# Performance work log

Hardware: AMD Instinct MI355X
Metric: run time of the kernel (lower is better)

The kernel has to match this reference:

```python
import jax, jax.numpy as jnp
import numpy as np


def setup_inputs() -> dict:
    key = jax.random.key(0)
    k1, k2 = jax.random.split(key)
    B, T, K, D = 8, 4096, 1024, 256
    x = jax.random.normal(k1, (B, T, D), dtype=jnp.float32)
    codebook = jax.random.normal(k2, (K, D), dtype=jnp.float32)
    return {"x": x, "codebook": codebook}


def reference(x, codebook):
    # Faithful to: dist = tf.norm(z_e - lookup_, axis=-1); argmin(dist, -1).
    # argmin of the Euclidean norm == argmin of the squared distance, so we
    # instead of materializing the (B, T, k, d) broadcast intermediate.
    x2 = jnp.sum(x * x, axis=-1, keepdims=True)          # (B, T, 1)
    c2 = jnp.sum(codebook * codebook, axis=-1)           # (k,)
    xc = jnp.einsum('btd,kd->btk', x, codebook)          # (B, T, k)
    dist2 = x2 + c2 - 2.0 * xc                           # (B, T, k)
    return jnp.argmin(dist2, axis=-1)                    # (B, T) int
```

## Files before the change

### kernel.cpp

```cpp
#include <hip/hip_runtime.h>
#include <stdint.h>

typedef __attribute__((ext_vector_type(8))) _Float16 f16x8;
typedef __attribute__((ext_vector_type(4))) float f32x4;

#define MARG 0.09375f

__device__ __forceinline__ void glds16(const void* g, void* l) {
  __builtin_amdgcn_global_load_lds(
      (const __attribute__((address_space(1))) void*)g,
      (__attribute__((address_space(3))) void*)l, 16, 0, 0);
}

__device__ __forceinline__ unsigned short f2h(float f) {
  return __builtin_bit_cast(unsigned short, (_Float16)f);
}

__global__ __launch_bounds__(256) void vq_prep_cb(const float* __restrict__ cb,
                                                  unsigned short* __restrict__ cbh,
                                                  float* __restrict__ hc,
                                                  float* __restrict__ cbT,
                                                  int* __restrict__ count) {
  __shared__ float tile[16][260];
  const int tid = threadIdx.x;
  const int r0 = blockIdx.x * 16;
  const int lane = tid & 63;
  const int wave = tid >> 6;

#pragma unroll
  for (int i = 0; i < 4; ++i) {
    int r = i * 4 + (tid >> 6);
    int d = lane * 4;
    float4 v = *reinterpret_cast<const float4*>(cb + (size_t)(r0 + r) * 256 + d);
    *reinterpret_cast<float4*>(&tile[r][d]) = v;
    ushort4 h;
    h.x = f2h(v.x); h.y = f2h(v.y); h.z = f2h(v.z); h.w = f2h(v.w);
    *reinterpret_cast<ushort4*>(cbh + (size_t)(r0 + r) * 256 + d) = h;
  }
  __syncthreads();

#pragma unroll
  for (int i = 0; i < 4; ++i) {
    int r = wave * 4 + i;
    float4 v = *reinterpret_cast<const float4*>(&tile[r][lane * 4]);
    float s = v.x * v.x + v.y * v.y + v.z * v.z + v.w * v.w;
#pragma unroll
    for (int m = 32; m >= 1; m >>= 1) s += __shfl_xor(s, m, 64);
    if (lane == 0) hc[r0 + r] = 0.5f * s;
  }

  {
    const int d = tid;
#pragma unroll
    for (int i = 0; i < 4; ++i) {
      float4 v = make_float4(tile[i * 4 + 0][d], tile[i * 4 + 1][d],
                             tile[i * 4 + 2][d], tile[i * 4 + 3][d]);
      *reinterpret_cast<float4*>(cbT + (size_t)d * 1024 + r0 + i * 4) = v;
    }
  }
  if (blockIdx.x == 0 && tid == 0) *count = 0;
}

__global__ __launch_bounds__(512, 4) void vq_mfma_kernel(
    const float* __restrict__ x, const unsigned short* __restrict__ cbh,
    const float* __restrict__ hc, int* __restrict__ out,
    int* __restrict__ list, int* __restrict__ count) {
  __shared__ unsigned short Alds[16384];
  __shared__ unsigned short Blds[16384];
  __shared__ float c2s[1024];
  __shared__ float cbv[4][64];
  __shared__ int   cbi[4][64];
  __shared__ float csv[4][64];

  const int tid = threadIdx.x;
  const int lane = tid & 63;
  const int wave = tid >> 6;
  const int wr = wave >> 2;
  const int wc = wave & 3;
  const int l15 = lane & 15;
  const int l4  = lane >> 4;
  const int bswz = (blockIdx.x & 7) * 64 + (blockIdx.x >> 3);
  const int r0 = bswz * 64;

  reinterpret_cast<float2*>(c2s)[tid] = reinterpret_cast<const float2*>(hc)[tid];

  {
    const int row = tid >> 3;
    const int cc  = tid & 7;
    const float* src = x + (size_t)(r0 + row) * 256 + cc * 32;
    unsigned short hv[32];
#pragma unroll
    for (int q = 0; q < 8; ++q) {
      float4 v = *reinterpret_cast<const float4*>(src + q * 4);
      hv[q * 4 + 0] = f2h(v.x); hv[q * 4 + 1] = f2h(v.y);
      hv[q * 4 + 2] = f2h(v.z); hv[q * 4 + 3] = f2h(v.w);
    }
    char* base = reinterpret_cast<char*>(Alds);
#pragma unroll
    for (int g = 0; g < 4; ++g) {
      int byte = (row * 512 + cc * 64 + g * 16) ^ ((row & 7) << 4);
      *reinterpret_cast<f16x8*>(base + byte) = *reinterpret_cast<const f16x8*>(&hv[g * 8]);
    }
  }

  auto stage = [&](int T1) {
    const int p = T1 & 1;
    const int n0 = (T1 >> 3) << 8;
    const int d0 = (T1 & 7) << 5;
    unsigned short* B = Blds + p * 8192;
#pragma unroll
    for (int r = 0; r < 2; ++r) {
      int idx = r * 512 + tid;
      int bch = (idx & 3) ^ ((idx >> 3) & 3);
      glds16(cbh + (size_t)(n0 + (idx >> 2)) * 256 + d0 + bch * 8, B + idx * 8);
    }
  };

  float bestv[2][4], secondv[2][4];
  int besti[2][4];
#pragma unroll
  for (int tr = 0; tr < 2; ++tr)
#pragma unroll
    for (int g = 0; g < 4; ++g) {
      bestv[tr][g] = -3.4e38f; secondv[tr][g] = -3.4e38f; besti[tr][g] = 0;
    }

  __syncthreads();
  stage(0);

  const int swzf = (l15 >> 1) & 3;
  int abase[2];
#pragma unroll
  for (int tr = 0; tr < 2; ++tr) {
    int arow = wr * 32 + tr * 16 + l15;
    abase[tr] = (arow * 512 + l4 * 16) ^ ((arow & 7) << 4);
  }

  int T = 0;
  for (int nt = 0; nt < 4; ++nt) {
    f32x4 acc[2][4];
#pragma unroll
    for (int tr = 0; tr < 2; ++tr)
#pragma unroll
      for (int tc = 0; tc < 4; ++tc) acc[tr][tc] = (f32x4){0.f, 0.f, 0.f, 0.f};

    for (int dt = 0; dt < 8; ++dt, ++T) {
      const int p = T & 1;
      if (T < 31) {
        stage(T + 1);
        asm volatile("s_waitcnt vmcnt(2)" ::: "memory");
      } else {
        asm volatile("s_waitcnt vmcnt(0)" ::: "memory");
      }
      __builtin_amdgcn_s_barrier();

      const char* Ab = reinterpret_cast<const char*>(Alds);
      const unsigned short* B = Blds + p * 8192;

      f16x8 af[2], bf[4];
#pragma unroll
      for (int tr = 0; tr < 2; ++tr)
        af[tr] = *reinterpret_cast<const f16x8*>(Ab + (abase[tr] ^ (dt * 64)));
#pragma unroll
      for (int tc = 0; tc < 4; ++tc) {
        int bcol = wc * 64 + tc * 16 + l15;
        bf[tc] = *reinterpret_cast<const f16x8*>(B + bcol * 32 + (l4 ^ swzf) * 8);
      }

#pragma unroll
      for (int tr = 0; tr < 2; ++tr)
#pragma unroll
        for (int tc = 0; tc < 4; ++tc)
          acc[tr][tc] = __builtin_amdgcn_mfma_f32_16x16x32_f16(af[tr], bf[tc], acc[tr][tc], 0, 0, 0);

      asm volatile("s_waitcnt lgkmcnt(0)" ::: "memory");
      __builtin_amdgcn_s_barrier();
    }

    const int cb0 = nt * 256 + wc * 64 + l15;
    float hcv[4];
#pragma unroll
    for (int tc = 0; tc < 4; ++tc) hcv[tc] = c2s[cb0 + tc * 16];
#pragma unroll
    for (int tr = 0; tr < 2; ++tr)
#pragma unroll
      for (int tc = 0; tc < 4; ++tc) {
        const int code = cb0 + tc * 16;
#pragma unroll
        for (int g = 0; g < 4; ++g) {
          float s = acc[tr][tc][g] - hcv[tc];
          bool gt = s > bestv[tr][g];
          float ns = gt ? bestv[tr][g] : fmaxf(secondv[tr][g], s);
          bestv[tr][g] = gt ? s : bestv[tr][g];
          besti[tr][g] = gt ? code : besti[tr][g];
          secondv[tr][g] = ns;
        }
      }
  }

#pragma unroll
  for (int tr = 0; tr < 2; ++tr)
#pragma unroll
    for (int g = 0; g < 4; ++g) {
      float bv = bestv[tr][g]; int bi = besti[tr][g]; float sv = secondv[tr][g];
#pragma unroll
      for (int m = 1; m < 16; m <<= 1) {
        float ov = __shfl_xor(bv, m, 64);
        int   oi = __shfl_xor(bi, m, 64);
        float os = __shfl_xor(sv, m, 64);
        sv = fmaxf(fmaxf(sv, os), fminf(bv, ov));
        bool gt = (ov > bv) || (ov == bv && oi < bi);
        bv = gt ? ov : bv;
        bi = gt ? oi : bi;
      }
      if (l15 == 0) {
        int rl = wr * 32 + tr * 16 + l4 * 4 + g;
        cbv[wc][rl] = bv; cbi[wc][rl] = bi; csv[wc][rl] = sv;
      }
    }

  __syncthreads();
  if (tid < 64) {
    float bv = cbv[0][tid]; int bi = cbi[0][tid]; float sv = csv[0][tid];
#pragma unroll
    for (int w2 = 1; w2 < 4; ++w2) {
      float ov = cbv[w2][tid]; int oi = cbi[w2][tid]; float os = csv[w2][tid];
      sv = fmaxf(fmaxf(sv, os), fminf(bv, ov));
      bool gt = (ov > bv) || (ov == bv && oi < bi);
      bv = gt ? ov : bv;
      bi = gt ? oi : bi;
    }
    out[r0 + tid] = bi;
    if (sv >= bv - MARG) {
      int slot = atomicAdd(count, 1);
      list[slot] = r0 + tid;
    }
  }
}

__global__ __launch_bounds__(512) void vq_cleanup(const float* __restrict__ x,
                                                  const float* __restrict__ cbT,
                                                  const float* __restrict__ hc,
                                                  const int* __restrict__ list,
                                                  const int* __restrict__ count,
                                                  int* __restrict__ out) {
  __shared__ float xt[4][256];
  __shared__ int rowids[4];
  __shared__ float wbv[8][2];
  __shared__ int   wbi[8][2];
  const int tid = threadIdx.x;
  const int wave = tid >> 6;
  const int half = tid >> 8;
  const int c0 = (tid & 255) * 4;
  const int n = *count;

  for (int t0 = blockIdx.x * 4; t0 < n; t0 += gridDim.x * 4) {
    __syncthreads();
    if (tid < 4) rowids[tid] = (t0 + tid < n) ? list[t0 + tid] : -1;
    __syncthreads();
    {
      int j = tid >> 7, seg = tid & 127;
      int row = rowids[j];
      if (row < 0) row = rowids[0];
      *reinterpret_cast<float2*>(&xt[j][seg * 2]) =
          *reinterpret_cast<const float2*>(x + (size_t)row * 256 + seg * 2);
    }
    __syncthreads();

    float a0[4], a1[4];
#pragma unroll
    for (int k = 0; k < 4; ++k) { a0[k] = 0.f; a1[k] = 0.f; }

    const float4* cvp = reinterpret_cast<const float4*>(cbT) + (c0 >> 2);
    const float* xr0 = &xt[half * 2 + 0][0];
    const float* xr1 = &xt[half * 2 + 1][0];
#pragma unroll 4
    for (int d = 0; d < 256; ++d) {
      float4 cv = cvp[d * 256];
      float x0 = xr0[d];
      float x1 = xr1[d];
      a0[0] = fmaf(cv.x, x0, a0[0]); a0[1] = fmaf(cv.y, x0, a0[1]);
      a0[2] = fmaf(cv.z, x0, a0[2]); a0[3] = fmaf(cv.w, x0, a0[3]);
      a1[0] = fmaf(cv.x, x1, a1[0]); a1[1] = fmaf(cv.y, x1, a1[1]);
      a1[2] = fmaf(cv.z, x1, a1[2]); a1[3] = fmaf(cv.w, x1, a1[3]);
    }

    float4 hcv = *reinterpret_cast<const float4*>(hc + c0);

#pragma unroll
    for (int r = 0; r < 2; ++r) {
      const float* a = (r == 0) ? a0 : a1;
      float bv = a[0] - hcv.x; int bi = c0;
      float s1 = a[1] - hcv.y; if (s1 > bv) { bv = s1; bi = c0 + 1; }
      float s2 = a[2] - hcv.z; if (s2 > bv) { bv = s2; bi = c0 + 2; }
      float s3 = a[3] - hcv.w; if (s3 > bv) { bv = s3; bi = c0 + 3; }
#pragma unroll
      for (int m = 1; m < 64; m <<= 1) {
        float ov = __shfl_xor(bv, m, 64);
        int   oi = __shfl_xor(bi, m, 64);
        bool gt = (ov > bv) || (ov == bv && oi < bi);
        bv = gt ? ov : bv;
        bi = gt ? oi : bi;
      }
      if ((tid & 63) == 0) { wbv[wave][r] = bv; wbi[wave][r] = bi; }
    }
    __syncthreads();
    if (tid < 4 && rowids[tid] >= 0) {
      int h2 = tid >> 1, lr = tid & 1;
      int wbase = h2 * 4;
      float bv = wbv[wbase][lr]; int bi = wbi[wbase][lr];
#pragma unroll
      for (int w2 = 1; w2 < 4; ++w2) {
        float ov = wbv[wbase + w2][lr]; int oi = wbi[wbase + w2][lr];
        if (ov > bv || (ov == bv && oi < bi)) { bv = ov; bi = oi; }
      }
      out[rowids[tid]] = bi;
    }
  }
}

#define BM 128
#define BN 256
#define BD 32
#define NT 512

__global__ __launch_bounds__(256) void vq_c2_kernel(const float* __restrict__ cb,
                                                    float* __restrict__ halfc2) {
  int row  = blockIdx.x * 4 + (threadIdx.x >> 6);
  int lane = threadIdx.x & 63;
  float4 v = *reinterpret_cast<const float4*>(cb + (size_t)row * 256 + lane * 4);
  float s = v.x * v.x + v.y * v.y + v.z * v.z + v.w * v.w;
#pragma unroll
  for (int m = 32; m >= 1; m >>= 1) s += __shfl_xor(s, m, 64);
  if (lane == 0) halfc2[row] = 0.5f * s;
}

__global__ __launch_bounds__(NT, 2) void vq_argmin_kernel(
    const float* __restrict__ x, const float* __restrict__ cb,
    const float* __restrict__ halfc2, int* __restrict__ out) {
  __shared__ float lds[2][(BM + BN) * BD];
  __shared__ float c2s[1024];
  const int tid = threadIdx.x;
  const int w   = tid >> 6;
  const int tc  = tid & 31;
  const int tr  = tid >> 5;
  const int r0  = blockIdx.x * BM;
  reinterpret_cast<float2*>(c2s)[tid] = reinterpret_cast<const float2*>(halfc2)[tid];
  const int sA  = tr & 7;
  const int sB  = tc & 7;
  const int sAB = sA ^ sB;
  const int cho = (((tid & 7) ^ w)) * 4;
  const int sub = tid >> 3;
  float bestv[8]; int besti[8];
#pragma unroll
  for (int i = 0; i < 8; ++i) { bestv[i] = -3.4e38f; besti[i] = 0; }
  auto stage = [&](int n0, int d0, int p) {
    float* dst  = &lds[p][0];
    float* dstB = dst + BM * BD;
#pragma unroll
    for (int r = 0; r < 2; ++r) {
      int t2 = r * NT + tid;
      glds16(x + (size_t)(r0 + r * 64 + sub) * 256 + d0 + cho, dst + t2 * 4);
    }
#pragma unroll
    for (int r = 0; r < 4; ++r) {
      int t2 = r * NT + tid;
      glds16(cb + (size_t)(n0 + r * 64 + sub) * 256 + d0 + cho, dstB + t2 * 4);
    }
  };
  stage(0, 0, 0);
  int t = 0;
  for (int nt = 0; nt < 4; ++nt) {
    float acc[8][8];
#pragma unroll
    for (int i = 0; i < 8; ++i)
#pragma unroll
      for (int j = 0; j < 8; ++j) acc[i][j] = 0.f;
    for (int dt = 0; dt < 8; ++dt, ++t) {
      const int p = t & 1;
      if (t < 31) {
        const int t1 = t + 1;
        stage((t1 >> 3) * BN, (t1 & 7) * BD, t1 & 1);
        asm volatile("s_waitcnt vmcnt(6)" ::: "memory");
      } else {
        asm volatile("s_waitcnt vmcnt(0)" ::: "memory");
      }
      __builtin_amdgcn_s_barrier();
      const float* pA = &lds[p][tr * 8 * BD];
      const float* pB = &lds[p][BM * BD + tc * 8 * BD];
#pragma unroll
      for (int cc = 0; cc < 8; ++cc) {
        const float* pBc = pB + ((cc ^ sAB) << 2);
        float4 a[8], b[8];
#pragma unroll
        for (int i = 0; i < 8; ++i)
          a[i] = *reinterpret_cast<const float4*>(pA + i * BD + cc * 4);
#pragma unroll
        for (int j = 0; j < 8; ++j)
          b[j] = *reinterpret_cast<const float4*>(pBc + j * BD);
#pragma unroll
        for (int i = 0; i < 8; ++i)
#pragma unroll
          for (int j = 0; j < 8; ++j) {
            acc[i][j] = fmaf(a[i].x, b[j].x, acc[i][j]);
            acc[i][j] = fmaf(a[i].y, b[j].y, acc[i][j]);
            acc[i][j] = fmaf(a[i].z, b[j].z, acc[i][j]);
            acc[i][j] = fmaf(a[i].w, b[j].w, acc[i][j]);
          }
      }
      asm volatile("s_waitcnt lgkmcnt(0)" ::: "memory");
      __builtin_amdgcn_s_barrier();
    }
    const int n0 = nt * BN;
#pragma unroll
    for (int j = 0; j < 8; ++j) {
      const int code = n0 + tc * 8 + j;
      const float hc = c2s[code];
#pragma unroll
      for (int i = 0; i < 8; ++i) {
        float s = acc[i][j] - hc;
        if (s > bestv[i]) { bestv[i] = s; besti[i] = code; }
      }
    }
  }
#pragma unroll
  for (int i = 0; i < 8; ++i) {
#pragma unroll
    for (int m = 1; m <= 16; m <<= 1) {
      float ov = __shfl_xor(bestv[i], m, 64);
      int   oi = __shfl_xor(besti[i], m, 64);
      if (ov > bestv[i] || (ov == bestv[i] && oi < besti[i])) { bestv[i] = ov; besti[i] = oi; }
    }
  }
  if (tc == 0) {
#pragma unroll
    for (int i = 0; i < 8; ++i) out[r0 + tr * 8 + i] = besti[i];
  }
}

extern "C" void kernel_launch(void* const* d_in, const int* in_sizes, int n_in,
                              void* d_out, int out_size, void* d_ws, size_t ws_size,
                              hipStream_t stream) {
  const float* x  = (const float*)d_in[0];
  const float* cb = (const float*)d_in[1];
  int* out = (int*)d_out;

  const size_t OFF_CH  = 0;
  const size_t OFF_HC  = OFF_CH + (size_t)1024 * 256 * 2;
  const size_t OFF_CBT = OFF_HC + (size_t)1024 * 4;
  const size_t OFF_LS  = OFF_CBT + (size_t)1024 * 256 * 4;
  const size_t OFF_CT  = OFF_LS + (size_t)32768 * 4;
  const size_t NEED    = OFF_CT + 64;

  if (ws_size >= NEED) {
    unsigned short* cbh = (unsigned short*)((char*)d_ws + OFF_CH);
    float* hc  = (float*)((char*)d_ws + OFF_HC);
    float* cbT = (float*)((char*)d_ws + OFF_CBT);
    int* list  = (int*)((char*)d_ws + OFF_LS);
    int* count = (int*)((char*)d_ws + OFF_CT);

    hipLaunchKernelGGL(vq_prep_cb, dim3(64), dim3(256), 0, stream, cb, cbh, hc, cbT, count);
    hipLaunchKernelGGL(vq_mfma_kernel, dim3(512), dim3(512), 0, stream,
                       x, cbh, hc, out, list, count);
    hipLaunchKernelGGL(vq_cleanup, dim3(1024), dim3(512), 0, stream,
                       x, cbT, hc, list, count, out);
  } else {
    float* c2 = (float*)d_ws;
    hipLaunchKernelGGL(vq_c2_kernel, dim3(256), dim3(256), 0, stream, cb, c2);
    hipLaunchKernelGGL(vq_argmin_kernel, dim3(32768 / BM), dim3(NT), 0, stream,
                       x, cb, c2, out);
  }
}
```

Before: 68.56 us.

## Give each wave a private codebook slice to drop per-step block barriers

Restructures the MFMA kernel so every wave handles all 64 rows against its own 128-code slice of the codebook, streamed into a per-wave double-buffered LDS region. Because each wave consumes only the data it staged itself, the two block-wide barriers per k-step go away and only vmcnt waits remain. The A tile is stored pre-fragmented in an MFMA-friendly layout, and the final reduction now merges eight waves instead of four. The catch is that each wave now reads more A fragments from LDS, register pressure rises (launch bounds drop to 2), and the fully unrolled loop grows code size.

```diff
diff --git a/kernel.cpp b/kernel.cpp
--- a/kernel.cpp
+++ b/kernel.cpp
@@ -61,22 +61,20 @@
   if (blockIdx.x == 0 && tid == 0) *count = 0;
 }
 
-__global__ __launch_bounds__(512, 4) void vq_mfma_kernel(
+__global__ __launch_bounds__(512, 2) void vq_mfma_kernel(
     const float* __restrict__ x, const unsigned short* __restrict__ cbh,
     const float* __restrict__ hc, int* __restrict__ out,
     int* __restrict__ list, int* __restrict__ count) {
   __shared__ unsigned short Alds[16384];
-  __shared__ unsigned short Blds[16384];
+  __shared__ unsigned short Bpriv[16384];
   __shared__ float c2s[1024];
-  __shared__ float cbv[4][64];
-  __shared__ int   cbi[4][64];
-  __shared__ float csv[4][64];
+  __shared__ float cbv[8][64];
+  __shared__ int   cbi[8][64];
+  __shared__ float csv[8][64];
 
   const int tid = threadIdx.x;
   const int lane = tid & 63;
   const int wave = tid >> 6;
-  const int wr = wave >> 2;
-  const int wc = wave & 3;
   const int l15 = lane & 15;
   const int l4  = lane >> 4;
   const int bswz = (blockIdx.x & 7) * 64 + (blockIdx.x >> 3);
@@ -96,113 +94,99 @@
       hv[q * 4 + 2] = f2h(v.z); hv[q * 4 + 3] = f2h(v.w);
     }
     char* base = reinterpret_cast<char*>(Alds);
+    const int rt = row >> 4, rl = row & 15;
+#pragma unroll
+    for (int j8 = 0; j8 < 4; ++j8) {
+      int byte = (rt * 8 + cc) * 1024 + j8 * 256 + rl * 16;
+      *reinterpret_cast<f16x8*>(base + byte) = *reinterpret_cast<const f16x8*>(&hv[j8 * 8]);
+    }
+  }
+  __syncthreads();
+
+  const char* Ab = reinterpret_cast<const char*>(Alds);
+  const int laneb = lane * 16;
+  char* Bw = reinterpret_cast<char*>(Bpriv) + wave * 4096;
+  const int cw0 = wave * 128;
+  const int bro = (l15 * 4 + l4) * 16;
+
+  auto stage = [&](int T) {
+    const int n0 = cw0 + ((T >> 3) << 5);
+    const int d0 = (T & 7) << 5;
+    char* dst = Bw + (T & 1) * 2048;
+    const unsigned short* s0 = cbh + (size_t)(n0 + (lane >> 2)) * 256 + d0 + ((lane & 3) << 3);
+    glds16(s0, dst + lane * 16);
+    glds16(s0 + 16 * 256, dst + 1024 + lane * 16);
+  };
+
+  float bestv[4][4], secv[4][4];
+  int besti[4][4];
+#pragma unroll
+  for (int rt = 0; rt < 4; ++rt)
 #pragma unroll
     for (int g = 0; g < 4; ++g) {
-      int byte = (row * 512 + cc * 64 + g * 16) ^ ((row & 7) << 4);
-      *reinterpret_cast<f16x8*>(base + byte) = *reinterpret_cast<const f16x8*>(&hv[g * 8]);
-    }
-  }
-
-  auto stage = [&](int T1) {
-    const int p = T1 & 1;
-    const int n0 = (T1 >> 3) << 8;
-    const int d0 = (T1 & 7) << 5;
-    unsigned short* B = Blds + p * 8192;
-#pragma unroll
-    for (int r = 0; r < 2; ++r) {
-      int idx = r * 512 + tid;
-      int bch = (idx & 3) ^ ((idx >> 3) & 3);
-      glds16(cbh + (size_t)(n0 + (idx >> 2)) * 256 + d0 + bch * 8, B + idx * 8);
-    }
-  };
-
-  float bestv[2][4], secondv[2][4];
-  int besti[2][4];
-#pragma unroll
-  for (int tr = 0; tr < 2; ++tr)
-#pragma unroll
-    for (int g = 0; g < 4; ++g) {
-      bestv[tr][g] = -3.4e38f; secondv[tr][g] = -3.4e38f; besti[tr][g] = 0;
-    }
-
-  __syncthreads();
+      bestv[rt][g] = -3.4e38f; secv[rt][g] = -3.4e38f; besti[rt][g] = 0;
+    }
+
   stage(0);
 
-  const int swzf = (l15 >> 1) & 3;
-  int abase[2];
-#pragma unroll
-  for (int tr = 0; tr < 2; ++tr) {
-    int arow = wr * 32 + tr * 16 + l15;
-    abase[tr] = (arow * 512 + l4 * 16) ^ ((arow & 7) << 4);
-  }
-
-  int T = 0;
-  for (int nt = 0; nt < 4; ++nt) {
-    f32x4 acc[2][4];
-#pragma unroll
-    for (int tr = 0; tr < 2; ++tr)
-#pragma unroll
-      for (int tc = 0; tc < 4; ++tc) acc[tr][tc] = (f32x4){0.f, 0.f, 0.f, 0.f};
-
-    for (int dt = 0; dt < 8; ++dt, ++T) {
-      const int p = T & 1;
+#pragma unroll
+  for (int cc = 0; cc < 4; ++cc) {
+    f32x4 acc[4][2];
+#pragma unroll
+    for (int rt = 0; rt < 4; ++rt)
+#pragma unroll
+      for (int ct = 0; ct < 2; ++ct) acc[rt][ct] = (f32x4){0.f, 0.f, 0.f, 0.f};
+
+#pragma unroll
+    for (int ks = 0; ks < 8; ++ks) {
+      const int T = cc * 8 + ks;
       if (T < 31) {
         stage(T + 1);
         asm volatile("s_waitcnt vmcnt(2)" ::: "memory");
       } else {
         asm volatile("s_waitcnt vmcnt(0)" ::: "memory");
       }
-      __builtin_amdgcn_s_barrier();
-
-      const char* Ab = reinterpret_cast<const char*>(Alds);
-      const unsigned short* B = Blds + p * 8192;
-
-      f16x8 af[2], bf[4];
-#pragma unroll
-      for (int tr = 0; tr < 2; ++tr)
-        af[tr] = *reinterpret_cast<const f16x8*>(Ab + (abase[tr] ^ (dt * 64)));
-#pragma unroll
-      for (int tc = 0; tc < 4; ++tc) {
-        int bcol = wc * 64 + tc * 16 + l15;
-        bf[tc] = *reinterpret_cast<const f16x8*>(B + bcol * 32 + (l4 ^ swzf) * 8);
-      }
-
-#pragma unroll
-      for (int tr = 0; tr < 2; ++tr)
-#pragma unroll
-        for (int tc = 0; tc < 4; ++tc)
-          acc[tr][tc] = __builtin_amdgcn_mfma_f32_16x16x32_f16(af[tr], bf[tc], acc[tr][tc], 0, 0, 0);
-
-      asm volatile("s_waitcnt lgkmcnt(0)" ::: "memory");
-      __builtin_amdgcn_s_barrier();
-    }
-
-    const int cb0 = nt * 256 + wc * 64 + l15;
-    float hcv[4];
-#pragma unroll
-    for (int tc = 0; tc < 4; ++tc) hcv[tc] = c2s[cb0 + tc * 16];
-#pragma unroll
-    for (int tr = 0; tr < 2; ++tr)
-#pragma unroll
-      for (int tc = 0; tc < 4; ++tc) {
-        const int code = cb0 + tc * 16;
+      const char* Bb = Bw + (T & 1) * 2048;
+
+      f16x8 afr[4], bfr[2];
+#pragma unroll
+      for (int rt = 0; rt < 4; ++rt)
+        afr[rt] = *reinterpret_cast<const f16x8*>(Ab + (rt * 8 + ks) * 1024 + laneb);
+#pragma unroll
+      for (int ct = 0; ct < 2; ++ct)
+        bfr[ct] = *reinterpret_cast<const f16x8*>(Bb + ct * 1024 + bro);
+
+#pragma unroll
+      for (int rt = 0; rt < 4; ++rt)
+#pragma unroll
+        for (int ct = 0; ct < 2; ++ct)
+          acc[rt][ct] = __builtin_amdgcn_mfma_f32_16x16x32_f16(
+              afr[rt], bfr[ct], acc[rt][ct], 0, 0, 0);
+    }
+
+#pragma unroll
+    for (int ct = 0; ct < 2; ++ct) {
+      const int code = cw0 + cc * 32 + ct * 16 + l15;
+      const float hcv = c2s[code];
+#pragma unroll
+      for (int rt = 0; rt < 4; ++rt)
 #pragma unroll
         for (int g = 0; g < 4; ++g) {
-          float s = acc[tr][tc][g] - hcv[tc];
-          bool gt = s > bestv[tr][g];
-          float ns = gt ? bestv[tr][g] : fmaxf(secondv[tr][g], s);
-          bestv[tr][g] = gt ? s : bestv[tr][g];
-          besti[tr][g] = gt ? code : besti[tr][g];
-          secondv[tr][g] = ns;
+          float sc = acc[rt][ct][g] - hcv;
+          bool gt = sc > bestv[rt][g];
+          float ns = gt ? bestv[rt][g] : fmaxf(secv[rt][g], sc);
+          bestv[rt][g] = gt ? sc : bestv[rt][g];
+          besti[rt][g] = gt ? code : besti[rt][g];
+          secv[rt][g] = ns;
         }
-      }
-  }
-
-#pragma unroll
-  for (int tr = 0; tr < 2; ++tr)
+    }
+  }
+
+#pragma unroll
+  for (int rt = 0; rt < 4; ++rt)
 #pragma unroll
     for (int g = 0; g < 4; ++g) {
-      float bv = bestv[tr][g]; int bi = besti[tr][g]; float sv = secondv[tr][g];
+      float bv = bestv[rt][g]; int bi = besti[rt][g]; float sv = secv[rt][g];
 #pragma unroll
       for (int m = 1; m < 16; m <<= 1) {
         float ov = __shfl_xor(bv, m, 64);
@@ -214,8 +198,8 @@
         bi = gt ? oi : bi;
       }
       if (l15 == 0) {
-        int rl = wr * 32 + tr * 16 + l4 * 4 + g;
-        cbv[wc][rl] = bv; cbi[wc][rl] = bi; csv[wc][rl] = sv;
+        int rl = rt * 16 + l4 * 4 + g;
+        cbv[wave][rl] = bv; cbi[wave][rl] = bi; csv[wave][rl] = sv;
       }
     }
 
@@ -223,7 +207,7 @@
   if (tid < 64) {
     float bv = cbv[0][tid]; int bi = cbi[0][tid]; float sv = csv[0][tid];
 #pragma unroll
-    for (int w2 = 1; w2 < 4; ++w2) {
+    for (int w2 = 1; w2 < 8; ++w2) {
       float ov = cbv[w2][tid]; int oi = cbi[w2][tid]; float os = csv[w2][tid];
       sv = fmaxf(fmaxf(sv, os), fminf(bv, ov));
       bool gt = (ov > bv) || (ov == bv && oi < bi);
```

Result: slower. 78.87 us (+15.0%).

## Pre-convert x to fp16 and stream A tiles via async LDS double buffering

Applied to the files above, without the earlier changes.

Adds a separate kernel that converts x to fp16 in workspace, then the MFMA kernel loads A slices per k-step with global_load_lds alongside the codebook tiles instead of converting a full resident A block up front. This shrinks LDS usage and removes the serial prologue conversion before the main loop. In exchange it adds an extra launch and a full fp16 write and reread of x through memory, and half the threads issue redundant A loads.

```diff
diff --git a/kernel.cpp b/kernel.cpp
--- a/kernel.cpp
+++ b/kernel.cpp
@@ -14,6 +14,18 @@
 
 __device__ __forceinline__ unsigned short f2h(float f) {
   return __builtin_bit_cast(unsigned short, (_Float16)f);
+}
+
+__global__ __launch_bounds__(256) void vq_prep_x(const float* __restrict__ x,
+                                                 unsigned short* __restrict__ xh) {
+  size_t base = ((size_t)blockIdx.x * 256 + threadIdx.x) * 16;
+#pragma unroll
+  for (int q = 0; q < 4; ++q) {
+    float4 v = *reinterpret_cast<const float4*>(x + base + q * 4);
+    ushort4 h;
+    h.x = f2h(v.x); h.y = f2h(v.y); h.z = f2h(v.z); h.w = f2h(v.w);
+    *reinterpret_cast<ushort4*>(xh + base + q * 4) = h;
+  }
 }
 
 __global__ __launch_bounds__(256) void vq_prep_cb(const float* __restrict__ cb,
@@ -62,11 +74,10 @@
 }
 
 __global__ __launch_bounds__(512, 4) void vq_mfma_kernel(
-    const float* __restrict__ x, const unsigned short* __restrict__ cbh,
+    const unsigned short* __restrict__ xh, const unsigned short* __restrict__ cbh,
     const float* __restrict__ hc, int* __restrict__ out,
     int* __restrict__ list, int* __restrict__ count) {
-  __shared__ unsigned short Alds[16384];
-  __shared__ unsigned short Blds[16384];
+  __shared__ unsigned short sm[20480];
   __shared__ float c2s[1024];
   __shared__ float cbv[4][64];
   __shared__ int   cbi[4][64];
@@ -84,30 +95,17 @@
 
   reinterpret_cast<float2*>(c2s)[tid] = reinterpret_cast<const float2*>(hc)[tid];
 
-  {
-    const int row = tid >> 3;
-    const int cc  = tid & 7;
-    const float* src = x + (size_t)(r0 + row) * 256 + cc * 32;
-    unsigned short hv[32];
-#pragma unroll
-    for (int q = 0; q < 8; ++q) {
-      float4 v = *reinterpret_cast<const float4*>(src + q * 4);
-      hv[q * 4 + 0] = f2h(v.x); hv[q * 4 + 1] = f2h(v.y);
-      hv[q * 4 + 2] = f2h(v.z); hv[q * 4 + 3] = f2h(v.w);
-    }
-    char* base = reinterpret_cast<char*>(Alds);
-#pragma unroll
-    for (int g = 0; g < 4; ++g) {
-      int byte = (row * 512 + cc * 64 + g * 16) ^ ((row & 7) << 4);
-      *reinterpret_cast<f16x8*>(base + byte) = *reinterpret_cast<const f16x8*>(&hv[g * 8]);
-    }
-  }
+  const int sA   = tid & 255;
+  const int srow = sA >> 2;
+  const int schA = (sA & 3) ^ ((sA >> 3) & 3);
 
   auto stage = [&](int T1) {
     const int p = T1 & 1;
     const int n0 = (T1 >> 3) << 8;
     const int d0 = (T1 & 7) << 5;
-    unsigned short* B = Blds + p * 8192;
+    unsigned short* A = sm + p * 2048;
+    unsigned short* B = sm + 4096 + p * 8192;
+    glds16(xh + (size_t)(r0 + srow) * 256 + d0 + schA * 8, A + sA * 8);
 #pragma unroll
     for (int r = 0; r < 2; ++r) {
       int idx = r * 512 + tid;
@@ -125,16 +123,9 @@
       bestv[tr][g] = -3.4e38f; secondv[tr][g] = -3.4e38f; besti[tr][g] = 0;
     }
 
-  __syncthreads();
   stage(0);
 
   const int swzf = (l15 >> 1) & 3;
-  int abase[2];
-#pragma unroll
-  for (int tr = 0; tr < 2; ++tr) {
-    int arow = wr * 32 + tr * 16 + l15;
-    abase[tr] = (arow * 512 + l4 * 16) ^ ((arow & 7) << 4);
-  }
 
   int T = 0;
   for (int nt = 0; nt < 4; ++nt) {
@@ -148,23 +139,25 @@
       const int p = T & 1;
       if (T < 31) {
         stage(T + 1);
-        asm volatile("s_waitcnt vmcnt(2)" ::: "memory");
+        asm volatile("s_waitcnt vmcnt(3)" ::: "memory");
       } else {
         asm volatile("s_waitcnt vmcnt(0)" ::: "memory");
       }
       __builtin_amdgcn_s_barrier();
 
-      const char* Ab = reinterpret_cast<const char*>(Alds);
-      const unsigned short* B = Blds + p * 8192;
+      const unsigned short* A = sm + p * 2048;
+      const unsigned short* B = sm + 4096 + p * 8192;
 
       f16x8 af[2], bf[4];
 #pragma unroll
-      for (int tr = 0; tr < 2; ++tr)
-        af[tr] = *reinterpret_cast<const f16x8*>(Ab + (abase[tr] ^ (dt * 64)));
+      for (int tr = 0; tr < 2; ++tr) {
+        int arow = wr * 32 + tr * 16 + l15;
+        af[tr] = *reinterpret_cast<const f16x8*>(A + arow * 32 + ((l4 ^ swzf) * 8));
+      }
 #pragma unroll
       for (int tc = 0; tc < 4; ++tc) {
         int bcol = wc * 64 + tc * 16 + l15;
-        bf[tc] = *reinterpret_cast<const f16x8*>(B + bcol * 32 + (l4 ^ swzf) * 8);
+        bf[tc] = *reinterpret_cast<const f16x8*>(B + bcol * 32 + ((l4 ^ swzf) * 8));
       }
 
 #pragma unroll
@@ -445,7 +438,8 @@
   const float* cb = (const float*)d_in[1];
   int* out = (int*)d_out;
 
-  const size_t OFF_CH  = 0;
+  const size_t OFF_XH  = 0;
+  const size_t OFF_CH  = OFF_XH + (size_t)32768 * 256 * 2;
   const size_t OFF_HC  = OFF_CH + (size_t)1024 * 256 * 2;
   const size_t OFF_CBT = OFF_HC + (size_t)1024 * 4;
   const size_t OFF_LS  = OFF_CBT + (size_t)1024 * 256 * 4;
@@ -453,15 +447,17 @@
   const size_t NEED    = OFF_CT + 64;
 
   if (ws_size >= NEED) {
+    unsigned short* xh  = (unsigned short*)((char*)d_ws + OFF_XH);
     unsigned short* cbh = (unsigned short*)((char*)d_ws + OFF_CH);
     float* hc  = (float*)((char*)d_ws + OFF_HC);
     float* cbT = (float*)((char*)d_ws + OFF_CBT);
     int* list  = (int*)((char*)d_ws + OFF_LS);
     int* count = (int*)((char*)d_ws + OFF_CT);
 
+    hipLaunchKernelGGL(vq_prep_x, dim3(2048), dim3(256), 0, stream, x, xh);
     hipLaunchKernelGGL(vq_prep_cb, dim3(64), dim3(256), 0, stream, cb, cbh, hc, cbT, count);
     hipLaunchKernelGGL(vq_mfma_kernel, dim3(512), dim3(512), 0, stream,
-                       x, cbh, hc, out, list, count);
+                       xh, cbh, hc, out, list, count);
     hipLaunchKernelGGL(vq_cleanup, dim3(1024), dim3(512), 0, stream,
                        x, cbT, hc, list, count, out);
   } else {
```

Result: slower. 79.11 us (+15.4%).
